# Optimization experiments

Measured on AMD Instinct MI355X. Metric: run time of the kernel, lower is better.

The kernel has to match this reference:

```python
import jax, jax.numpy as jnp
import numpy as np

B = 64; SEQ = 512; PRED = 96; D = 321; HID = 2048
WIN = 64; STRIDE = WIN // 2; FT = WIN // 2 + 1
LOW = int(FT * 0.3); MID = int(FT * 0.4); HIGH = FT - LOW - MID  # 9, 13, 11
NW = SEQ // STRIDE + 1; EMBED = NW * WIN  # 17, 1088
EPS = 1e-5; SCALE = 0.02
LH = int(LOW * 2.0); MH = int(MID * 2.0); HH = int(HIGH * 2.0)  # 18, 26, 22


def _clayer(key, fan_in, fan_out):
    k1, k2, k3, k4 = jax.random.split(key, 4)
    return (jax.random.normal(k1, (fan_in, fan_out), jnp.float32) * SCALE,
            jax.random.normal(k2, (fan_in, fan_out), jnp.float32) * SCALE,
            jax.random.normal(k3, (fan_out,), jnp.float32) * SCALE,
            jax.random.normal(k4, (fan_out,), jnp.float32) * SCALE)


def setup_inputs() -> dict:
    key = jax.random.key(0)
    ks = jax.random.split(key, 12)
    inp = {}
    inp["x"] = jax.random.normal(ks[0], (B, SEQ, D), jnp.float32)
    inp["x_mark_enc"] = jax.random.normal(ks[1], (B, SEQ, 4), jnp.float32)
    inp["x_dec"] = jax.random.normal(ks[2], (B, PRED, D), jnp.float32)
    inp["x_mark_dec"] = jax.random.normal(ks[3], (B, PRED, 4), jnp.float32)
    n = jnp.arange(WIN, dtype=jnp.float32)
    inp["window"] = 0.5 * (1.0 - jnp.cos(2.0 * jnp.pi * n / WIN))  # torch.hann_window (periodic)
    inp["revin_w"] = jnp.ones((D,), jnp.float32)
    inp["revin_b"] = jnp.zeros((D,), jnp.float32)
    # low band filter: 3 complex layers LOW->LH->LH->LOW
    for i, (fi, fo) in enumerate([(LOW, LH), (LH, LH), (LH, LOW)]):
        wr, wi, br, bi = _clayer(jax.random.fold_in(ks[4], i), fi, fo)
        inp[f"low{i}_wr"], inp[f"low{i}_wi"], inp[f"low{i}_br"], inp[f"low{i}_bi"] = wr, wi, br, bi
    # mid band filter: 2 complex layers MID->MH->MID
    for i, (fi, fo) in enumerate([(MID, MH), (MH, MID)]):
        wr, wi, br, bi = _clayer(jax.random.fold_in(ks[5], i), fi, fo)
        inp[f"mid{i}_wr"], inp[f"mid{i}_wi"], inp[f"mid{i}_br"], inp[f"mid{i}_bi"] = wr, wi, br, bi
    # high band filter: 1 complex layer HIGH->HIGH
    wr, wi, br, bi = _clayer(ks[6], HIGH, HIGH)
    inp["high0_wr"], inp["high0_wi"], inp["high0_br"], inp["high0_bi"] = wr, wi, br, bi
    inp["fc1_w"] = jax.random.normal(ks[7], (EMBED, HID), jnp.float32) * SCALE
    inp["fc1_b"] = jnp.zeros((HID,), jnp.float32)
    inp["fc2_w"] = jax.random.normal(ks[8], (HID, PRED), jnp.float32) * SCALE
    inp["fc2_b"] = jnp.zeros((PRED,), jnp.float32)
    return inp


def _clin(z, wr, wi, br, bi):
    return z @ (wr + 1j * wi) + (br + 1j * bi)


def _cact(z):
    return jax.nn.leaky_relu(z.real) + 1j * jax.nn.leaky_relu(z.imag)


def reference(x, x_mark_enc, x_dec, x_mark_dec, window, revin_w, revin_b,
              low0_wr, low0_wi, low0_br, low0_bi,
              low1_wr, low1_wi, low1_br, low1_bi,
              low2_wr, low2_wi, low2_br, low2_bi,
              mid0_wr, mid0_wi, mid0_br, mid0_bi,
              mid1_wr, mid1_wi, mid1_br, mid1_bi,
              high0_wr, high0_wi, high0_br, high0_bi,
              fc1_w, fc1_b, fc2_w, fc2_b):
    # RevIN norm over time dim
    mean = jnp.mean(x, axis=1, keepdims=True)
    std = jnp.sqrt(jnp.var(x, axis=1, keepdims=True) + EPS)
    xn = (x - mean) / std * revin_w + revin_b
    xc = jnp.transpose(xn, (0, 2, 1))                      # [B, D, L]
    xp = jnp.pad(xc, ((0, 0), (0, 0), (STRIDE, STRIDE)))
    # batched window extraction (replaces python loop over windows)
    idx = jnp.arange(NW)[:, None] * STRIDE + jnp.arange(WIN)[None, :]
    seg = xp[:, :, idx]
    w = window / jnp.linalg.norm(window)
    xf = jnp.fft.rfft(seg * w, axis=-1)                    # [B, D, NW, FT] complex
    low = xf[..., :LOW]
    mid = xf[..., LOW:LOW + MID]
    high = xf[..., LOW + MID:]
    low = _clin(_cact(_clin(_cact(_clin(low, low0_wr, low0_wi, low0_br, low0_bi)),
                            low1_wr, low1_wi, low1_br, low1_bi)),
                low2_wr, low2_wi, low2_br, low2_bi)
    mid = _clin(_cact(_clin(mid, mid0_wr, mid0_wi, mid0_br, mid0_bi)),
                mid1_wr, mid1_wi, mid1_br, mid1_bi)
    high = _clin(high, high0_wr, high0_wi, high0_br, high0_bi)
    xfil = jnp.concatenate([low, mid, high], axis=-1)      # [B, D, NW, FT]
    xt = jnp.fft.irfft(xfil, n=WIN, axis=-1)
    emb = xt.reshape(x.shape[0], D, EMBED)
    h = jax.nn.leaky_relu(emb @ fc1_w + fc1_b)
    y = h @ fc2_w + fc2_b                                  # [B, D, PRED]
    y = jnp.transpose(y, (0, 2, 1))                        # [B, PRED, D]
    # RevIN denorm
    y = (y - revin_b) / (revin_w + EPS * EPS) * std + mean
    return y
```

## Files before the change

### kernel.cpp

```cpp
#include <hip/hip_runtime.h>

typedef unsigned short u16;
typedef unsigned int   u32;
typedef __attribute__((ext_vector_type(4))) float  fvec4;
typedef __attribute__((ext_vector_type(8))) __bf16 bvec8;

#define NB    64
#define SEQL  512
#define DCH   321
#define BDTOT (NB * DCH)
#define NWIN  17
#define PREDL 96
#define MWTOT (BDTOT * NWIN)
#define KPAD  1152

__device__ __forceinline__ u16 f2bf(float f) {
    union { float f; u32 u; } v; v.f = f;
    u32 r = v.u + 0x7FFFu + ((v.u >> 16) & 1u);
    return (u16)(r >> 16);
}
__device__ __forceinline__ float lrelu(float v) { return v > 0.f ? v : 0.01f * v; }

__device__ __forceinline__ void gld16(const u16* g, u16* l) {
    __builtin_amdgcn_global_load_lds((const __attribute__((address_space(1))) void*)g,
                                     (__attribute__((address_space(3))) void*)l, 16, 0, 0);
}

__global__ __launch_bounds__(256) void stats_kernel(const float* __restrict__ x,
                                                    float* __restrict__ mean,
                                                    float* __restrict__ rstd,
                                                    float* __restrict__ stdv) {
    __shared__ float ls[2][4][64];
    int i = threadIdx.x & 63;
    int j = threadIdx.x >> 6;
    int bd = blockIdx.x * 64 + i;
    int b = bd / DCH, d = bd - b * DCH;
    float s = 0.f, ss = 0.f;
    for (int t = j; t < SEQL; t += 4) {
        float v = x[((size_t)b * SEQL + t) * DCH + d];
        s += v; ss += v * v;
    }
    ls[0][j][i] = s; ls[1][j][i] = ss;
    __syncthreads();
    if (j == 0) {
        s  = ls[0][0][i] + ls[0][1][i] + ls[0][2][i] + ls[0][3][i];
        ss = ls[1][0][i] + ls[1][1][i] + ls[1][2][i] + ls[1][3][i];
        float m   = s * (1.f / SEQL);
        float var = ss * (1.f / SEQL) - m * m;
        float st  = sqrtf(var + 1e-5f);
        mean[bd] = m; rstd[bd] = 1.f / st; stdv[bd] = st;
    }
}

__global__ __launch_bounds__(256) void norm_transpose(const float* __restrict__ x,
                                                      const float* __restrict__ mean,
                                                      const float* __restrict__ rstd,
                                                      const float* __restrict__ rw,
                                                      const float* __restrict__ rb,
                                                      u16* __restrict__ xnT) {
    __shared__ float tile[64][65];
    int d0 = blockIdx.x * 64, s0 = blockIdx.y * 64, b = blockIdx.z;
    for (int e = threadIdx.x; e < 4096; e += 256) {
        int sr = e >> 6, dc = e & 63;
        int d = d0 + dc;
        tile[sr][dc] = (d < DCH) ? x[((size_t)b * SEQL + s0 + sr) * DCH + d] : 0.f;
    }
    __syncthreads();
    for (int e = threadIdx.x; e < 4096; e += 256) {
        int dr = e >> 6, sc = e & 63;
        int d = d0 + dr;
        if (d < DCH) {
            int bd = b * DCH + d;
            float v = (tile[sc][dr] - mean[bd]) * rstd[bd] * rw[d] + rb[d];
            xnT[(size_t)bd * 576 + 32 + s0 + sc] = f2bf(v);
        }
    }
}

__global__ __launch_bounds__(256) void pads(u16* __restrict__ xnT, u16* __restrict__ EMB) {
    int idx = blockIdx.x * 256 + threadIdx.x;
    if (idx < BDTOT * 64) {
        int bd = idx >> 6, q = idx & 63;
        int off = q < 32 ? q : 512 + q;
        xnT[(size_t)bd * 576 + off] = 0;
    } else if (idx < BDTOT * 64 + BDTOT * 8) {
        int t = idx - BDTOT * 64;
        int bd = t >> 3, o = (t & 7) * 8;
        fvec4 z = {0.f, 0.f, 0.f, 0.f};
        *(fvec4*)&EMB[(size_t)bd * KPAD + 1088 + o] = z;
    }
}

__global__ __launch_bounds__(256) void precompute_kernel(
    const float* __restrict__ window,
    const float* __restrict__ l0wr, const float* __restrict__ l0wi,
    const float* __restrict__ l0br, const float* __restrict__ l0bi,
    const float* __restrict__ l1wr, const float* __restrict__ l1wi,
    const float* __restrict__ l1br, const float* __restrict__ l1bi,
    const float* __restrict__ l2wr, const float* __restrict__ l2wi,
    const float* __restrict__ l2br, const float* __restrict__ l2bi,
    const float* __restrict__ m0wr, const float* __restrict__ m0wi,
    const float* __restrict__ m0br, const float* __restrict__ m0bi,
    const float* __restrict__ m1wr, const float* __restrict__ m1wi,
    const float* __restrict__ m1br, const float* __restrict__ m1bi,
    const float* __restrict__ h0wr, const float* __restrict__ h0wi,
    const float* __restrict__ h0br, const float* __restrict__ h0bi,
    u16* __restrict__ A1t, u16* __restrict__ W1t, u16* __restrict__ B2t,
    float* __restrict__ bias1, float* __restrict__ bias2, float* __restrict__ biast)
{
    int idx = blockIdx.x * 256 + threadIdx.x;
    float nrm = 0.f;
    for (int i = 0; i < 64; ++i) nrm += window[i] * window[i];
    float inv = 1.0f / sqrtf(nrm);
    const float STEP = 6.283185307179586f / 64.f;
    auto Cc = [&](int n, int k) { return  window[n] * inv * cosf(STEP * (float)((k * n) & 63)); };
    auto Ss = [&](int n, int k) { return -window[n] * inv * sinf(STEP * (float)((k * n) & 63)); };
    auto aRe = [&](int k, int n) {
        float sc = (k == 0 || k == 32) ? (1.f / 64.f) : (2.f / 64.f);
        return sc * cosf(STEP * (float)((k * n) & 63));
    };
    auto aIm = [&](int k, int n) {
        if (k == 0 || k == 32) return 0.f;
        return -(2.f / 64.f) * sinf(STEP * (float)((k * n) & 63));
    };
    if (idx < 16384) {
        int j = idx >> 6, n = idx & 63;
        float v = 0.f;
        if (j < 18)                    { for (int k = 0; k < 9;  ++k) v += Cc(n,k)   *l0wr[k*18+j]      - Ss(n,k)   *l0wi[k*18+j]; }
        else if (j < 36)               { int jj=j-18; for (int k = 0; k < 9;  ++k) v += Cc(n,k)   *l0wi[k*18+jj] + Ss(n,k)   *l0wr[k*18+jj]; }
        else if (j >= 64  && j < 90)   { int jj=j-64; for (int k = 0; k < 13; ++k) v += Cc(n,9+k) *m0wr[k*26+jj] - Ss(n,9+k) *m0wi[k*26+jj]; }
        else if (j >= 90  && j < 116)  { int jj=j-90; for (int k = 0; k < 13; ++k) v += Cc(n,9+k) *m0wi[k*26+jj] + Ss(n,9+k) *m0wr[k*26+jj]; }
        else if (j >= 128 && j < 139)  { int jj=j-128;for (int k = 0; k < 11; ++k) v += Cc(n,22+k)*h0wr[k*11+jj] - Ss(n,22+k)*h0wi[k*11+jj]; }
        else if (j >= 139 && j < 150)  { int jj=j-139;for (int k = 0; k < 11; ++k) v += Cc(n,22+k)*h0wi[k*11+jj] + Ss(n,22+k)*h0wr[k*11+jj]; }
        A1t[idx] = f2bf(v);
    } else if (idx < 24576) {
        int t = idx - 16384; int j = t >> 6, k = t & 63;
        float v = 0.f;
        if (j < 18)      { if (k < 18) v = l1wr[k*18+j];        else if (k < 36) v = -l1wi[(k-18)*18+j]; }
        else if (j < 36) { int jj=j-18; if (k < 18) v = l1wi[k*18+jj]; else if (k < 36) v =  l1wr[(k-18)*18+jj]; }
        W1t[t] = f2bf(v);
    } else if (idx < 49152) {
        int t = idx - 24576; int n = t / 192, c = t - n * 192;
        float v = 0.f;
        if (n < 64) {
            if (c < 18)                  { for (int m = 0; m < 9;  ++m) v +=  l2wr[c*9+m]     *aRe(m,n)   + l2wi[c*9+m]     *aIm(m,n); }
            else if (c < 36)             { int cc=c-18; for (int m = 0; m < 9;  ++m) v += -l2wi[cc*9+m]   *aRe(m,n)   + l2wr[cc*9+m]   *aIm(m,n); }
            else if (c >= 64 && c < 90)  { int cc=c-64; for (int m = 0; m < 13; ++m) v +=  m1wr[cc*13+m]  *aRe(9+m,n) + m1wi[cc*13+m]  *aIm(9+m,n); }
            else if (c >= 90 && c < 116) { int cc=c-90; for (int m = 0; m < 13; ++m) v += -m1wi[cc*13+m]  *aRe(9+m,n) + m1wr[cc*13+m]  *aIm(9+m,n); }
            else if (c >= 128 && c < 139){ v = aRe(22 + (c-128), n); }
            else if (c >= 139 && c < 150){ v = aIm(22 + (c-139), n); }
        }
        B2t[t] = f2bf(v);
    } else if (idx < 49344) {
        int c = idx - 49152;
        float v = 0.f;
        if (c < 18) v = l0br[c];
        else if (c < 36) v = l0bi[c-18];
        else if (c >= 64 && c < 90) v = m0br[c-64];
        else if (c >= 90 && c < 116) v = m0bi[c-90];
        bias1[c] = v;
    } else if (idx < 49472) {
        int c = idx - 49344;
        float v = 0.f;
        if (c < 18) v = l1br[c]; else if (c < 36) v = l1bi[c-18];
        bias2[c] = v;
    } else if (idx < 49536) {
        int n = idx - 49472;
        float v = 0.f;
        for (int k = 0; k <= 32; ++k) {
            float br = (k < 9) ? l2br[k] : (k < 22 ? m1br[k-9] : h0br[k-22]);
            float bi = (k < 9) ? l2bi[k] : (k < 22 ? m1bi[k-9] : h0bi[k-22]);
            v += aRe(k, n) * br + aIm(k, n) * bi;
        }
        biast[n] = v;
    }
}

__global__ __launch_bounds__(256) void wtrans(const float* __restrict__ W, u16* __restrict__ Wt,
                                              int R, int C, int Cpad, int ldw) {
    __shared__ float t[32][33];
    int c0 = blockIdx.x * 32, r0 = blockIdx.y * 32;
    for (int e = threadIdx.x; e < 1024; e += 256) {
        int rr = e >> 5, cc = e & 31;
        int rg = r0 + rr, cg = c0 + cc;
        t[rr][cc] = (rg < R && cg < C) ? W[(size_t)rg * C + cg] : 0.f;
    }
    __syncthreads();
    for (int e = threadIdx.x; e < 1024; e += 256) {
        int cr = e >> 5, rc = e & 31;
        int cg = c0 + cr, rg = r0 + rc;
        if (cg < Cpad && rg < ldw) Wt[(size_t)cg * ldw + rg] = f2bf(t[rc][cr]);
    }
}

__global__ __launch_bounds__(256) void spectral_fused(
    const u16* __restrict__ xnT, const u16* __restrict__ A1t,
    const u16* __restrict__ W1t, const u16* __restrict__ B2t,
    const float* __restrict__ bias1, const float* __restrict__ bias2,
    const float* __restrict__ biast, u16* __restrict__ EMB)
{
    __shared__ u16 XB[64 * 72];
    __shared__ u16 ACT[64 * 208];
    const int tid  = threadIdx.x;
    const int lane = tid & 63;
    const int wn   = tid >> 6;
    const int r0   = blockIdx.x * 64;

    {
        int rr = tid >> 2;
        int cc = (tid & 3) * 16;
        u32 gr = (u32)(r0 + rr);
        u32 bd = gr / 17u, nw = gr - bd * 17u;
        const u16* src = xnT + (size_t)bd * 576 + nw * 32 + cc;
        *(bvec8*)&XB[rr * 72 + cc]     = *(const bvec8*)(src);
        *(bvec8*)&XB[rr * 72 + cc + 8] = *(const bvec8*)(src + 8);
    }
    __syncthreads();

    fvec4 acc1[4][3] = {};
#pragma unroll
    for (int kk = 0; kk < 2; ++kk) {
        int ko = kk * 32 + ((lane >> 4) << 3);
        bvec8 af[4], bf[3];
#pragma unroll
        for (int m = 0; m < 4; ++m)
            af[m] = *(const bvec8*)&XB[(m * 16 + (lane & 15)) * 72 + ko];
#pragma unroll
        for (int n = 0; n < 3; ++n)
            bf[n] = *(const bvec8*)(A1t + (size_t)(wn * 48 + n * 16 + (lane & 15)) * 64 + ko);
#pragma unroll
        for (int m = 0; m < 4; ++m)
#pragma unroll
            for (int n = 0; n < 3; ++n)
                acc1[m][n] = __builtin_amdgcn_mfma_f32_16x16x32_bf16(af[m], bf[n], acc1[m][n], 0, 0, 0);
    }
#pragma unroll
    for (int n = 0; n < 3; ++n) {
        int col = wn * 48 + n * 16 + (lane & 15);
        float bs = bias1[col];
#pragma unroll
        for (int m = 0; m < 4; ++m)
#pragma unroll
            for (int q = 0; q < 4; ++q) {
                int row = m * 16 + ((lane >> 4) << 2) + q;
                float v = acc1[m][n][q] + bs;
                if (col < 128) v = lrelu(v);
                ACT[row * 208 + col] = f2bf(v);
            }
    }
    __syncthreads();

    fvec4 acc2[4] = {};
#pragma unroll
    for (int kk = 0; kk < 2; ++kk) {
        int ko = kk * 32 + ((lane >> 4) << 3);
        bvec8 bf = *(const bvec8*)(W1t + (size_t)(wn * 16 + (lane & 15)) * 64 + ko);
#pragma unroll
        for (int m = 0; m < 4; ++m) {
            bvec8 af = *(const bvec8*)&ACT[(m * 16 + (lane & 15)) * 208 + ko];
            acc2[m] = __builtin_amdgcn_mfma_f32_16x16x32_bf16(af, bf, acc2[m], 0, 0, 0);
        }
    }
    __syncthreads();
    {
        int col = wn * 16 + (lane & 15);
        float bs = bias2[col];
#pragma unroll
        for (int m = 0; m < 4; ++m)
#pragma unroll
            for (int q = 0; q < 4; ++q) {
                int row = m * 16 + ((lane >> 4) << 2) + q;
                ACT[row * 208 + col] = f2bf(lrelu(acc2[m][q] + bs));
            }
    }
    __syncthreads();

    fvec4 acc3[4] = {};
#pragma unroll
    for (int kk = 0; kk < 6; ++kk) {
        int ko = kk * 32 + ((lane >> 4) << 3);
        bvec8 bf = *(const bvec8*)(B2t + (size_t)(wn * 16 + (lane & 15)) * 192 + ko);
#pragma unroll
        for (int m = 0; m < 4; ++m) {
            bvec8 af = *(const bvec8*)&ACT[(m * 16 + (lane & 15)) * 208 + ko];
            acc3[m] = __builtin_amdgcn_mfma_f32_16x16x32_bf16(af, bf, acc3[m], 0, 0, 0);
        }
    }
    {
        int col = wn * 16 + (lane & 15);
        float bs = biast[col];
#pragma unroll
        for (int m = 0; m < 4; ++m)
#pragma unroll
            for (int q = 0; q < 4; ++q) {
                int row = m * 16 + ((lane >> 4) << 2) + q;
                int wr = r0 + row;
                int bd2 = wr / 17, nw2 = wr - bd2 * 17;
                EMB[(size_t)bd2 * KPAD + nw2 * 64 + col] = f2bf(acc3[m][q] + bs);
            }
    }
}

template <int SWZ>
__global__ __launch_bounds__(512, 2) void gemm_fused(
    const u16* __restrict__ A, const u16* __restrict__ Bt,
    const float* __restrict__ bias, const u16* __restrict__ W2t,
    float* __restrict__ YP,
    int Mloc, int K, long long a_off, int nwg)
{
    extern __shared__ u16 lds[];
    const int tid  = threadIdx.x;
    const int lane = tid & 63;
    const int l15  = lane & 15;
    const int hi   = lane >> 4;
    const int wid  = tid >> 6;
    const int wm   = wid >> 2;
    const int wn   = wid & 3;
    int wg;
    if (SWZ) {
        int bid = blockIdx.x;
        int q = nwg >> 3, r = nwg & 7, xcd = bid & 7, off = bid >> 3;
        wg = (xcd < r) ? (xcd * (q + 1) + off) : (r * (q + 1) + (xcd - r) * q + off);
    } else wg = blockIdx.x;
    const int mt = wg >> 3;
    const int nt = wg & 7;
    const int bm0 = mt * 256, bn0 = nt * 256;

    const u16* sbase[4][2];
#pragma unroll
    for (int u = 0; u < 4; ++u) {
#pragma unroll
        for (int j = 0; j < 2; ++j) {
            int idx = j * 512 + tid;
            if ((u & 1) == 0) {
                int row = (u >> 1) * 128 + (idx >> 3);
                int kc = ((idx & 7) ^ (row & 7)) << 3;
                int rl = bm0 + row; if (rl > Mloc - 1) rl = Mloc - 1;
                sbase[u][j] = A + (size_t)(a_off + rl) * K + kc;
            } else {
                int row = idx >> 2;
                int kc = (u >> 1) * 32 + (((idx & 3) ^ ((row >> 1) & 3)) << 3);
                sbase[u][j] = Bt + (size_t)(bn0 + row) * K + kc;
            }
        }
    }
    auto stage_unit = [&](int bufb, int tg, int u) {
        int base = ((u & 1) == 0) ? ((u >> 1) * 8192) : (16384 + (u >> 1) * 8192);
        u16* dstb = lds + bufb * 32768 + base;
#pragma unroll
        for (int j = 0; j < 2; ++j) {
            int idx = j * 512 + tid;
            gld16(sbase[u][j] + ((size_t)tg << 6), dstb + idx * 8);
        }
    };

    fvec4 acc[8][4] = {};
    const int NT = K >> 6;

    stage_unit(0, 0, 0); stage_unit(0, 0, 1); stage_unit(0, 0, 2); stage_unit(0, 0, 3);
    asm volatile("s_waitcnt vmcnt(4)");
    __builtin_amdgcn_s_barrier();

    for (int t = 0; t < NT; ++t) {
        const int cur = t & 1;
        const u16* Ab = lds + cur * 32768;
        const u16* Bb = Ab + 16384;
        const bool nl = (t < NT - 1);
        bvec8 bfr[4];
#pragma unroll
        for (int p = 0; p < 4; ++p) {
            const int kk = p >> 1, mh = p & 1;
            bvec8 af[4];
            if (mh == 0) {
#pragma unroll
                for (int n = 0; n < 4; ++n) {
                    int r = wn * 64 + n * 16 + l15;
                    int ch = hi ^ ((r >> 1) & 3);
                    bfr[n] = *(const bvec8*)&Bb[kk * 8192 + r * 32 + ch * 8];
                }
            }
#pragma unroll
            for (int mm = 0; mm < 4; ++mm) {
                int r = mh * 128 + wm * 64 + mm * 16 + l15;
                int ch = (kk * 4 + hi) ^ (r & 7);
                af[mm] = *(const bvec8*)&Ab[r * 64 + ch * 8];
            }
            if (nl) stage_unit(cur ^ 1, t + 1, p);
            __builtin_amdgcn_s_barrier();
            asm volatile("s_waitcnt lgkmcnt(0)");
            __builtin_amdgcn_s_setprio(1);
#pragma unroll
            for (int mm = 0; mm < 4; ++mm)
#pragma unroll
                for (int n = 0; n < 4; ++n)
                    acc[mh * 4 + mm][n] = __builtin_amdgcn_mfma_f32_16x16x32_bf16(
                        af[mm], bfr[n], acc[mh * 4 + mm][n], 0, 0, 0);
            __builtin_amdgcn_s_setprio(0);
            if (p == 0) {
                if (nl) asm volatile("s_waitcnt vmcnt(4)");
                else    asm volatile("s_waitcnt vmcnt(2)");
            } else if (p == 1) {
                if (nl) asm volatile("s_waitcnt vmcnt(4)");
                else    asm volatile("s_waitcnt vmcnt(0)");
            } else if (p == 3) {
                if (nl) asm volatile("s_waitcnt vmcnt(4)");
            }
            __builtin_amdgcn_s_barrier();
        }
    }

#pragma unroll
    for (int m = 0; m < 8; ++m) {
        int mh = m >> 2, mm = m & 3;
        int row0 = mh * 128 + wm * 64 + mm * 16 + hi * 4;
#pragma unroll
        for (int n = 0; n < 4; ++n) {
            int col = wn * 64 + n * 16 + l15;
            float bs = bias[bn0 + col];
#pragma unroll
            for (int q = 0; q < 4; ++q) {
                int r = row0 + q;
                lds[r * 256 + (((col >> 3) ^ (r & 7)) << 3) + (col & 7)] =
                    f2bf(lrelu(acc[m][n][q] + bs));
            }
        }
    }
    __syncthreads();

    fvec4 acc2[2][6] = {};
    const int wr0 = wid * 32;
#pragma unroll
    for (int ks = 0; ks < 8; ++ks) {
        bvec8 bw[6];
#pragma unroll
        for (int cf = 0; cf < 6; ++cf)
            bw[cf] = *(const bvec8*)(W2t + (size_t)(cf * 16 + l15) * 2048 + bn0 + ks * 32 + hi * 8);
#pragma unroll
        for (int rf = 0; rf < 2; ++rf) {
            int r = wr0 + rf * 16 + l15;
            bvec8 ah = *(const bvec8*)&lds[r * 256 + (((ks * 4 + hi) ^ (r & 7)) << 3)];
#pragma unroll
            for (int cf = 0; cf < 6; ++cf)
                acc2[rf][cf] = __builtin_amdgcn_mfma_f32_16x16x32_bf16(ah, bw[cf], acc2[rf][cf], 0, 0, 0);
        }
    }
    float* yp = YP + (size_t)nt * ((size_t)BDTOT * PREDL);
#pragma unroll
    for (int rf = 0; rf < 2; ++rf) {
#pragma unroll
        for (int cf = 0; cf < 6; ++cf) {
#pragma unroll
            for (int q = 0; q < 4; ++q) {
                int r = bm0 + wr0 + rf * 16 + hi * 4 + q;
                if (r < Mloc) yp[(size_t)r * PREDL + cf * 16 + l15] = acc2[rf][cf][q];
            }
        }
    }
}

__global__ __launch_bounds__(256) void final_denorm(const float* __restrict__ YP,
                                                    const float* __restrict__ fc2b,
                                                    const float* __restrict__ mean,
                                                    const float* __restrict__ stdv,
                                                    const float* __restrict__ rw,
                                                    const float* __restrict__ rb,
                                                    float* __restrict__ out) {
    const size_t PART = (size_t)BDTOT * PREDL;
    __shared__ float t[32][33];
    int d0 = blockIdx.x * 32, p0 = blockIdx.y * 32, b = blockIdx.z;
    for (int e = threadIdx.x; e < 1024; e += 256) {
        int di = e >> 5, pj = e & 31;
        int d = d0 + di, p = p0 + pj;
        if (d < DCH && p < PREDL) {
            size_t off = ((size_t)b * DCH + d) * PREDL + p;
            float s = fc2b[p];
#pragma unroll
            for (int i = 0; i < 8; ++i) s += YP[off + (size_t)i * PART];
            t[di][pj] = s;
        } else t[di][pj] = 0.f;
    }
    __syncthreads();
    for (int e = threadIdx.x; e < 1024; e += 256) {
        int pi = e >> 5, dj = e & 31;
        int d = d0 + dj, p = p0 + pi;
        if (d < DCH && p < PREDL) {
            int bd = b * DCH + d;
            float v = (t[dj][pi] - rb[d]) / (rw[d] + 1e-10f) * stdv[bd] + mean[bd];
            out[((size_t)b * PREDL + p) * DCH + d] = v;
        }
    }
}

extern "C" void kernel_launch(void* const* d_in, const int* in_sizes, int n_in,
                              void* d_out, int out_size, void* d_ws, size_t ws_size,
                              hipStream_t stream) {
    const float* x      = (const float*)d_in[0];
    const float* window = (const float*)d_in[4];
    const float* rw     = (const float*)d_in[5];
    const float* rb     = (const float*)d_in[6];
    const float* l0wr = (const float*)d_in[7],  *l0wi = (const float*)d_in[8];
    const float* l0br = (const float*)d_in[9],  *l0bi = (const float*)d_in[10];
    const float* l1wr = (const float*)d_in[11], *l1wi = (const float*)d_in[12];
    const float* l1br = (const float*)d_in[13], *l1bi = (const float*)d_in[14];
    const float* l2wr = (const float*)d_in[15], *l2wi = (const float*)d_in[16];
    const float* l2br = (const float*)d_in[17], *l2bi = (const float*)d_in[18];
    const float* m0wr = (const float*)d_in[19], *m0wi = (const float*)d_in[20];
    const float* m0br = (const float*)d_in[21], *m0bi = (const float*)d_in[22];
    const float* m1wr = (const float*)d_in[23], *m1wi = (const float*)d_in[24];
    const float* m1br = (const float*)d_in[25], *m1bi = (const float*)d_in[26];
    const float* h0wr = (const float*)d_in[27], *h0wi = (const float*)d_in[28];
    const float* h0br = (const float*)d_in[29], *h0bi = (const float*)d_in[30];
    const float* fc1w = (const float*)d_in[31];
    const float* fc1b = (const float*)d_in[32];
    const float* fc2w = (const float*)d_in[33];
    const float* fc2b = (const float*)d_in[34];

    char* p = (char*)d_ws;
    auto alloc = [&](size_t n) { char* r = p; p += (n + 255) & ~(size_t)255; return r; };
    float* mean  = (float*)alloc(BDTOT * 4);
    float* rstd  = (float*)alloc(BDTOT * 4);
    float* stdv  = (float*)alloc(BDTOT * 4);
    float* bias1 = (float*)alloc(192 * 4);
    float* bias2 = (float*)alloc(128 * 4);
    float* biast = (float*)alloc(64 * 4);
    u16* A1t   = (u16*)alloc(256 * 64 * 2);
    u16* W1t   = (u16*)alloc(128 * 64 * 2);
    u16* B2t   = (u16*)alloc(128 * 192 * 2);
    u16* fc1wT = (u16*)alloc((size_t)2048 * KPAD * 2);
    u16* fc2wT = (u16*)alloc((size_t)128 * 2048 * 2);
    u16* xnT   = (u16*)alloc((size_t)BDTOT * 576 * 2);
    u16* EMB   = (u16*)alloc((size_t)BDTOT * KPAD * 2);
    float* YP  = (float*)alloc((size_t)8 * BDTOT * PREDL * 4);

    hipFuncSetAttribute(reinterpret_cast<const void*>(&gemm_fused<1>),
                        hipFuncAttributeMaxDynamicSharedMemorySize, 131072);

    dim3 blk(256);
    stats_kernel<<<BDTOT / 64, blk, 0, stream>>>(x, mean, rstd, stdv);
    norm_transpose<<<dim3(6, 8, NB), blk, 0, stream>>>(x, mean, rstd, rw, rb, xnT);
    pads<<<(BDTOT * 72 + 255) / 256, blk, 0, stream>>>(xnT, EMB);
    precompute_kernel<<<194, blk, 0, stream>>>(window,
        l0wr, l0wi, l0br, l0bi, l1wr, l1wi, l1br, l1bi, l2wr, l2wi, l2br, l2bi,
        m0wr, m0wi, m0br, m0bi, m1wr, m1wi, m1br, m1bi, h0wr, h0wi, h0br, h0bi,
        A1t, W1t, B2t, bias1, bias2, biast);
    wtrans<<<dim3(64, 36), blk, 0, stream>>>(fc1w, fc1wT, 1088, 2048, 2048, KPAD);
    wtrans<<<dim3(4, 64),  blk, 0, stream>>>(fc2w, fc2wT, 2048, 96, 128, 2048);

    spectral_fused<<<MWTOT / 64, blk, 0, stream>>>(xnT, A1t, W1t, B2t, bias1, bias2, biast, EMB);

    {
        int gm = (BDTOT + 255) / 256;
        int nwg = 8 * gm;
        gemm_fused<1><<<dim3(nwg), dim3(512), 131072, stream>>>(EMB, fc1wT, fc1b, fc2wT, YP,
            BDTOT, KPAD, 0, nwg);
    }
    final_denorm<<<dim3(11, 3, NB), blk, 0, stream>>>(YP, fc2b, mean, stdv, rw, rb, (float*)d_out);
}
```

Baseline: 295.3 us.

## Fuse RevIN stats with normalize-transpose, repad ACT, restructure GEMM K-loop prefetch

```diff
diff --git a/kernel.cpp b/kernel.cpp
--- a/kernel.cpp
+++ b/kernel.cpp
@@ -26,54 +26,53 @@
                                      (__attribute__((address_space(3))) void*)l, 16, 0, 0);
 }
 
-__global__ __launch_bounds__(256) void stats_kernel(const float* __restrict__ x,
-                                                    float* __restrict__ mean,
-                                                    float* __restrict__ rstd,
-                                                    float* __restrict__ stdv) {
-    __shared__ float ls[2][4][64];
-    int i = threadIdx.x & 63;
-    int j = threadIdx.x >> 6;
-    int bd = blockIdx.x * 64 + i;
-    int b = bd / DCH, d = bd - b * DCH;
+__global__ __launch_bounds__(256) void norm_stats_fused(
+    const float* __restrict__ x, const float* __restrict__ rw,
+    const float* __restrict__ rb, float* __restrict__ mean,
+    float* __restrict__ stdv, u16* __restrict__ xnT) {
+    __shared__ float red[2][4][64];
+    __shared__ float tile[64][65];
+    __shared__ float sm[64], sa[64], sb2[64];
+    const int tid = threadIdx.x;
+    const int i = tid & 63, j = tid >> 6;
+    const int d0 = blockIdx.x * 64, b = blockIdx.y;
+    const int d = d0 + i;
+    const bool dok = d < DCH;
     float s = 0.f, ss = 0.f;
-    for (int t = j; t < SEQL; t += 4) {
-        float v = x[((size_t)b * SEQL + t) * DCH + d];
-        s += v; ss += v * v;
-    }
-    ls[0][j][i] = s; ls[1][j][i] = ss;
-    __syncthreads();
-    if (j == 0) {
-        s  = ls[0][0][i] + ls[0][1][i] + ls[0][2][i] + ls[0][3][i];
-        ss = ls[1][0][i] + ls[1][1][i] + ls[1][2][i] + ls[1][3][i];
+    if (dok) {
+        for (int t = j; t < SEQL; t += 4) {
+            float v = x[((size_t)b * SEQL + t) * DCH + d];
+            s += v; ss += v * v;
+        }
+    }
+    red[0][j][i] = s; red[1][j][i] = ss;
+    __syncthreads();
+    if (j == 0 && dok) {
+        s  = red[0][0][i] + red[0][1][i] + red[0][2][i] + red[0][3][i];
+        ss = red[1][0][i] + red[1][1][i] + red[1][2][i] + red[1][3][i];
         float m   = s * (1.f / SEQL);
         float var = ss * (1.f / SEQL) - m * m;
         float st  = sqrtf(var + 1e-5f);
-        mean[bd] = m; rstd[bd] = 1.f / st; stdv[bd] = st;
-    }
-}
-
-__global__ __launch_bounds__(256) void norm_transpose(const float* __restrict__ x,
-                                                      const float* __restrict__ mean,
-                                                      const float* __restrict__ rstd,
-                                                      const float* __restrict__ rw,
-                                                      const float* __restrict__ rb,
-                                                      u16* __restrict__ xnT) {
-    __shared__ float tile[64][65];
-    int d0 = blockIdx.x * 64, s0 = blockIdx.y * 64, b = blockIdx.z;
-    for (int e = threadIdx.x; e < 4096; e += 256) {
-        int sr = e >> 6, dc = e & 63;
-        int d = d0 + dc;
-        tile[sr][dc] = (d < DCH) ? x[((size_t)b * SEQL + s0 + sr) * DCH + d] : 0.f;
-    }
-    __syncthreads();
-    for (int e = threadIdx.x; e < 4096; e += 256) {
-        int dr = e >> 6, sc = e & 63;
-        int d = d0 + dr;
-        if (d < DCH) {
-            int bd = b * DCH + d;
-            float v = (tile[sc][dr] - mean[bd]) * rstd[bd] * rw[d] + rb[d];
-            xnT[(size_t)bd * 576 + 32 + s0 + sc] = f2bf(v);
-        }
+        int bd = b * DCH + d;
+        mean[bd] = m; stdv[bd] = st;
+        sm[i] = m; sa[i] = rw[d] / st; sb2[i] = rb[d];
+    }
+    __syncthreads();
+    for (int sc = 0; sc < 8; ++sc) {
+        for (int e = tid; e < 4096; e += 256) {
+            int sr = e >> 6, dc = e & 63;
+            tile[sr][dc] = (d0 + dc < DCH)
+                ? x[((size_t)b * SEQL + sc * 64 + sr) * DCH + d0 + dc] : 0.f;
+        }
+        __syncthreads();
+        for (int e = tid; e < 4096; e += 256) {
+            int dr = e >> 6, scol = e & 63;
+            if (d0 + dr < DCH) {
+                float v = (tile[scol][dr] - sm[dr]) * sa[dr] + sb2[dr];
+                xnT[((size_t)b * DCH + d0 + dr) * 576 + 32 + sc * 64 + scol] = f2bf(v);
+            }
+        }
+        __syncthreads();
     }
 }
 
@@ -200,7 +199,7 @@
     const float* __restrict__ biast, u16* __restrict__ EMB)
 {
     __shared__ u16 XB[64 * 72];
-    __shared__ u16 ACT[64 * 208];
+    __shared__ u16 ACT[64 * 200];
     const int tid  = threadIdx.x;
     const int lane = tid & 63;
     const int wn   = tid >> 6;
@@ -245,7 +244,7 @@
                 int row = m * 16 + ((lane >> 4) << 2) + q;
                 float v = acc1[m][n][q] + bs;
                 if (col < 128) v = lrelu(v);
-                ACT[row * 208 + col] = f2bf(v);
+                ACT[row * 200 + col] = f2bf(v);
             }
     }
     __syncthreads();
@@ -257,7 +256,7 @@
         bvec8 bf = *(const bvec8*)(W1t + (size_t)(wn * 16 + (lane & 15)) * 64 + ko);
 #pragma unroll
         for (int m = 0; m < 4; ++m) {
-            bvec8 af = *(const bvec8*)&ACT[(m * 16 + (lane & 15)) * 208 + ko];
+            bvec8 af = *(const bvec8*)&ACT[(m * 16 + (lane & 15)) * 200 + ko];
             acc2[m] = __builtin_amdgcn_mfma_f32_16x16x32_bf16(af, bf, acc2[m], 0, 0, 0);
         }
     }
@@ -270,7 +269,7 @@
 #pragma unroll
             for (int q = 0; q < 4; ++q) {
                 int row = m * 16 + ((lane >> 4) << 2) + q;
-                ACT[row * 208 + col] = f2bf(lrelu(acc2[m][q] + bs));
+                ACT[row * 200 + col] = f2bf(lrelu(acc2[m][q] + bs));
             }
     }
     __syncthreads();
@@ -282,7 +281,7 @@
         bvec8 bf = *(const bvec8*)(B2t + (size_t)(wn * 16 + (lane & 15)) * 192 + ko);
 #pragma unroll
         for (int m = 0; m < 4; ++m) {
-            bvec8 af = *(const bvec8*)&ACT[(m * 16 + (lane & 15)) * 208 + ko];
+            bvec8 af = *(const bvec8*)&ACT[(m * 16 + (lane & 15)) * 200 + ko];
             acc3[m] = __builtin_amdgcn_mfma_f32_16x16x32_bf16(af, bf, acc3[m], 0, 0, 0);
         }
     }
@@ -356,20 +355,24 @@
 
     fvec4 acc[8][4] = {};
     const int NT = K >> 6;
+    const int NPAIR = NT >> 1;
 
     stage_unit(0, 0, 0); stage_unit(0, 0, 1); stage_unit(0, 0, 2); stage_unit(0, 0, 3);
+    stage_unit(1, 1, 1); stage_unit(1, 1, 0);
     asm volatile("s_waitcnt vmcnt(4)");
     __builtin_amdgcn_s_barrier();
 
-    for (int t = 0; t < NT; ++t) {
-        const int cur = t & 1;
-        const u16* Ab = lds + cur * 32768;
-        const u16* Bb = Ab + 16384;
-        const bool nl = (t < NT - 1);
+    for (int pr = 0; pr < NPAIR; ++pr) {
+        const bool hasT2 = (2 * pr + 2 < NT);
+        const bool hasT3 = (2 * pr + 3 < NT);
         bvec8 bfr[4];
 #pragma unroll
-        for (int p = 0; p < 4; ++p) {
+        for (int ph = 0; ph < 8; ++ph) {
+            const int tb = ph >> 2;
+            const int p  = ph & 3;
             const int kk = p >> 1, mh = p & 1;
+            const u16* Ab = lds + tb * 32768;
+            const u16* Bb = Ab + 16384;
             bvec8 af[4];
             if (mh == 0) {
 #pragma unroll
@@ -385,7 +388,14 @@
                 int ch = (kk * 4 + hi) ^ (r & 7);
                 af[mm] = *(const bvec8*)&Ab[r * 64 + ch * 8];
             }
-            if (nl) stage_unit(cur ^ 1, t + 1, p);
+            if (ph == 0)      stage_unit(1, 2 * pr + 1, 2);
+            else if (ph == 1) stage_unit(1, 2 * pr + 1, 3);
+            else if (ph == 2) { if (hasT2) stage_unit(0, 2 * pr + 2, 1); }
+            else if (ph == 3) { if (hasT2) stage_unit(0, 2 * pr + 2, 0); }
+            else if (ph == 4) { if (hasT2) stage_unit(0, 2 * pr + 2, 2); }
+            else if (ph == 5) { if (hasT2) stage_unit(0, 2 * pr + 2, 3); }
+            else if (ph == 6) { if (hasT3) stage_unit(1, 2 * pr + 3, 1); }
+            else              { if (hasT3) stage_unit(1, 2 * pr + 3, 0); }
             __builtin_amdgcn_s_barrier();
             asm volatile("s_waitcnt lgkmcnt(0)");
             __builtin_amdgcn_s_setprio(1);
@@ -396,14 +406,11 @@
                     acc[mh * 4 + mm][n] = __builtin_amdgcn_mfma_f32_16x16x32_bf16(
                         af[mm], bfr[n], acc[mh * 4 + mm][n], 0, 0, 0);
             __builtin_amdgcn_s_setprio(0);
-            if (p == 0) {
-                if (nl) asm volatile("s_waitcnt vmcnt(4)");
-                else    asm volatile("s_waitcnt vmcnt(2)");
-            } else if (p == 1) {
-                if (nl) asm volatile("s_waitcnt vmcnt(4)");
-                else    asm volatile("s_waitcnt vmcnt(0)");
-            } else if (p == 3) {
-                if (nl) asm volatile("s_waitcnt vmcnt(4)");
+            if (ph == 3) {
+                if (hasT2) asm volatile("s_waitcnt vmcnt(4)");
+                else       asm volatile("s_waitcnt vmcnt(0)");
+            } else if (ph == 7) {
+                if (hasT3) asm volatile("s_waitcnt vmcnt(4)");
             }
             __builtin_amdgcn_s_barrier();
         }
@@ -518,7 +525,6 @@
     char* p = (char*)d_ws;
     auto alloc = [&](size_t n) { char* r = p; p += (n + 255) & ~(size_t)255; return r; };
     float* mean  = (float*)alloc(BDTOT * 4);
-    float* rstd  = (float*)alloc(BDTOT * 4);
     float* stdv  = (float*)alloc(BDTOT * 4);
     float* bias1 = (float*)alloc(192 * 4);
     float* bias2 = (float*)alloc(128 * 4);
@@ -536,8 +542,7 @@
                         hipFuncAttributeMaxDynamicSharedMemorySize, 131072);
 
     dim3 blk(256);
-    stats_kernel<<<BDTOT / 64, blk, 0, stream>>>(x, mean, rstd, stdv);
-    norm_transpose<<<dim3(6, 8, NB), blk, 0, stream>>>(x, mean, rstd, rw, rb, xnT);
+    norm_stats_fused<<<dim3(6, NB), blk, 0, stream>>>(x, rw, rb, mean, stdv, xnT);
     pads<<<(BDTOT * 72 + 255) / 256, blk, 0, stream>>>(xnT, EMB);
     precompute_kernel<<<194, blk, 0, stream>>>(window,
         l0wr, l0wi, l0br, l0bi, l1wr, l1wi, l1br, l1bi, l2wr, l2wi, l2br, l2bi,
```

New measurement: 317.7 us. 1.08x slower.
